# Kernel optimization log

Hardware: AMD Instinct MI355X
Metric: run time of the kernel (lower is better)

The kernel has to match this reference:

```python
import jax, jax.numpy as jnp
import numpy as np

DIM = 256          # inter_dim
GROUPS = 32        # GroupNorm groups
P = 8              # patch_size (square)
EPS = 1e-5


def group_norm(x, gamma, beta):
    # x: (b, c, h, w); normalize over (c/G, h, w) per group, biased variance (torch default)
    b, c, h, w = x.shape
    xg = x.reshape(b, GROUPS, -1)
    m = xg.mean(-1, keepdims=True)
    v = xg.var(-1, keepdims=True)
    xn = ((xg - m) * jax.lax.rsqrt(v + EPS)).reshape(b, c, h, w)
    return xn * gamma[None, :, None, None] + beta[None, :, None, None]


def to_patches(x):
    # 'b c (h p1) (w p2) -> (b h w) c (p1 p2)'
    b, c, H, W = x.shape
    nh, nw = H // P, W // P
    x = x.reshape(b, c, nh, P, nw, P).transpose(0, 2, 4, 1, 3, 5)  # b nh nw c p1 p2
    return x.reshape(b * nh * nw, c, P * P)


def from_patches(x, b, H, W):
    # '(b h w) c (p1 p2) -> b c (h p1) (w p2)'
    nh, nw = H // P, W // P
    c = x.shape[1]
    x = x.reshape(b, nh, nw, c, P, P).transpose(0, 3, 1, 4, 2, 5)
    return x.reshape(b, c, H, W)


def setup_inputs() -> dict:
    key = jax.random.key(0)
    ks = jax.random.split(key, 4)
    b, c, H, W = 8, 256, 128, 128
    return {
        "x_low": jax.random.normal(ks[0], (b, c, H, W), jnp.float32),
        "x_high": jax.random.normal(ks[1], (b, c, H, W), jnp.float32),
        "wq": jax.random.normal(ks[2], (DIM, c), jnp.float32) * (1.0 / np.sqrt(c)),
        "wk": jax.random.normal(ks[3], (DIM, c), jnp.float32) * (1.0 / np.sqrt(c)),
        "gq": jnp.ones((DIM,), jnp.float32),
        "bq": jnp.zeros((DIM,), jnp.float32),
        "gk": jnp.ones((DIM,), jnp.float32),
        "bk": jnp.zeros((DIM,), jnp.float32),
    }


def reference(x_low, x_high, wq, wk, gq, bq, gk, bk):
    b, c, H, W = x_low.shape
    # 1x1 conv (bias-free) + GroupNorm for q and k projections
    q = group_norm(jnp.einsum('oc,bchw->bohw', wq, x_low), gq, bq)
    k = group_norm(jnp.einsum('oc,bchw->bohw', wk, x_high), gk, bk)
    qp = to_patches(q).transpose(0, 2, 1)   # (n_windows, p, c)
    kp = to_patches(k)                      # (n_windows, c, p)
    attn = jax.nn.softmax(jnp.matmul(qp, kp) / jnp.sqrt(jnp.float32(DIM)), axis=-1)  # (n, p, p)
    out = jnp.matmul(attn, kp.transpose(0, 2, 1))  # (n, p, c)
    out = from_patches(out.transpose(0, 2, 1), b, H, W)
    return out + x_low
```

## Files before the change

### kernel.cpp

```cpp
#include <hip/hip_runtime.h>
#include <hip/hip_bf16.h>

using short8 = __attribute__((ext_vector_type(8))) short;
using fx4    = __attribute__((ext_vector_type(4))) float;

#define NB 8
#define CDIM 256
#define HH 128
#define NPIX 16384
#define NG_ELEMS 131072.0f

__device__ __forceinline__ float bf2f(short s) {
    union { unsigned u; float f; } c; c.u = ((unsigned)(unsigned short)s) << 16; return c.f;
}
__device__ __forceinline__ short f2bf(float f) {
    union { float f; unsigned u; } c; c.f = f;
    unsigned u = c.u;
    u += 0x7FFFu + ((u >> 16) & 1u);
    return (short)(u >> 16);
}
__device__ __forceinline__ short2 f2bf2(float a, float b) {
    __hip_bfloat162 h = __float22bfloat162_rn(make_float2(a, b));
    union { __hip_bfloat162 b; short2 s; } c; c.b = h; return c.s;
}

__global__ __launch_bounds__(256) void kW(const float* __restrict__ wq,
                                          const float* __restrict__ wk,
                                          short* __restrict__ WB) {
    int kc = blockIdx.x;
    int t  = blockIdx.y;
    const float* W = t ? wk : wq;
    int tid = threadIdx.x;
    int ntile = tid >> 4, lr = tid & 15;
    int n = ntile * 16 + lr;
#pragma unroll
    for (int quad = 0; quad < 4; ++quad) {
        const float* p = W + (size_t)n * CDIM + kc * 32 + quad * 8;
        fx4 v0 = *(const fx4*)p;
        fx4 v1 = *(const fx4*)(p + 4);
        union { short8 v; short2 h[4]; } s;
        s.h[0] = f2bf2(v0[0], v0[1]);
        s.h[1] = f2bf2(v0[2], v0[3]);
        s.h[2] = f2bf2(v1[0], v1[1]);
        s.h[3] = f2bf2(v1[2], v1[3]);
        *(short8*)(WB + ((((size_t)t * 8 + kc) * 16 + ntile) * 64 + quad * 16 + lr) * 8) = s.v;
    }
}

__global__ __launch_bounds__(256, 2) void kG(const float* __restrict__ xlo,
                                             const float* __restrict__ xhi,
                                             const short* __restrict__ WB,
                                             short* __restrict__ qt,
                                             short* __restrict__ kt,
                                             float* __restrict__ stats) {
    int m0 = blockIdx.x * 128;
    int zy = blockIdx.y;
    int b = zy >> 1, t = zy & 1;
    const float* X = (t ? xhi : xlo) + (size_t)b * CDIM * NPIX;
    const short* WBt = WB + (size_t)t * 8 * 16 * 64 * 8;
    short* OUT = (t ? kt : qt) + (size_t)b * NPIX * CDIM;
    int tid = threadIdx.x;
    int w = tid >> 6, l = tid & 63, lr = l & 15, quad = l >> 4;
    int mh = w >> 1, nh = w & 1;
    int pixb = m0 + mh * 64 + lr;

    fx4 acc[4][8];
#pragma unroll
    for (int mt = 0; mt < 4; ++mt)
#pragma unroll
        for (int nt = 0; nt < 8; ++nt) { acc[mt][nt][0]=0.f; acc[mt][nt][1]=0.f; acc[mt][nt][2]=0.f; acc[mt][nt][3]=0.f; }

    for (int kc = 0; kc < 8; ++kc) {
        short8 bf[8];
        const short* wb = WBt + ((size_t)kc * 16 + nh * 8) * 64 * 8 + (size_t)l * 8;
#pragma unroll
        for (int nt = 0; nt < 8; ++nt)
            bf[nt] = *(const short8*)(wb + (size_t)nt * 64 * 8);
        short8 af[4];
        const float* xp = X + (size_t)(kc * 32 + quad * 8) * NPIX + pixb;
#pragma unroll
        for (int mt = 0; mt < 4; ++mt) {
            float e0 = xp[(size_t)0 * NPIX + mt * 16];
            float e1 = xp[(size_t)1 * NPIX + mt * 16];
            float e2 = xp[(size_t)2 * NPIX + mt * 16];
            float e3 = xp[(size_t)3 * NPIX + mt * 16];
            float e4 = xp[(size_t)4 * NPIX + mt * 16];
            float e5 = xp[(size_t)5 * NPIX + mt * 16];
            float e6 = xp[(size_t)6 * NPIX + mt * 16];
            float e7 = xp[(size_t)7 * NPIX + mt * 16];
            union { short8 v; short2 h[4]; } s;
            s.h[0] = f2bf2(e0, e1); s.h[1] = f2bf2(e2, e3);
            s.h[2] = f2bf2(e4, e5); s.h[3] = f2bf2(e6, e7);
            af[mt] = s.v;
        }
#pragma unroll
        for (int mt = 0; mt < 4; ++mt)
#pragma unroll
            for (int nt = 0; nt < 8; ++nt)
                acc[mt][nt] = __builtin_amdgcn_mfma_f32_16x16x32_bf16(af[mt], bf[nt], acc[mt][nt], 0, 0, 0);
    }

#pragma unroll
    for (int nt = 0; nt < 8; ++nt) {
        float s = 0.f, ss = 0.f;
#pragma unroll
        for (int mt = 0; mt < 4; ++mt)
#pragma unroll
            for (int r = 0; r < 4; ++r) { float v = acc[mt][nt][r]; s += v; ss += v * v; }
        s += __shfl_xor(s, 16); ss += __shfl_xor(ss, 16);
        s += __shfl_xor(s, 32); ss += __shfl_xor(ss, 32);
        s += __shfl_xor(s, 1);  ss += __shfl_xor(ss, 1);
        s += __shfl_xor(s, 2);  ss += __shfl_xor(ss, 2);
        s += __shfl_xor(s, 4);  ss += __shfl_xor(ss, 4);
        if (l == 0 || l == 8) {
            int o = nh * 128 + nt * 16 + (l & 15);
            int g = o >> 3;
            float* st = stats + ((size_t)(t * NB + b) * 32 + g) * 2;
            atomicAdd(st, s);
            atomicAdd(st + 1, ss);
        }
    }

#pragma unroll
    for (int mt = 0; mt < 4; ++mt) {
        int pix = m0 + mh * 64 + mt * 16 + quad * 4;
#pragma unroll
        for (int nt = 0; nt < 8; ++nt) {
            int o = nh * 128 + nt * 16 + lr;
            short2 p0 = f2bf2(acc[mt][nt][0], acc[mt][nt][1]);
            short2 p1 = f2bf2(acc[mt][nt][2], acc[mt][nt][3]);
            OUT[(size_t)(pix + 0) * CDIM + o] = p0.x;
            OUT[(size_t)(pix + 1) * CDIM + o] = p0.y;
            OUT[(size_t)(pix + 2) * CDIM + o] = p1.x;
            OUT[(size_t)(pix + 3) * CDIM + o] = p1.y;
        }
    }
}

__global__ __launch_bounds__(256) void kS(const float* __restrict__ stats,
                                          const float* __restrict__ gq,
                                          const float* __restrict__ bq,
                                          const float* __restrict__ gk,
                                          const float* __restrict__ bk,
                                          float* __restrict__ scale,
                                          float* __restrict__ shift) {
    int id = blockIdx.x * 256 + threadIdx.x;
    int t = id >> 11, b = (id >> 8) & 7, o = id & 255;
    int g = o >> 3;
    const float* st = stats + ((size_t)(t * NB + b) * 32 + g) * 2;
    float mean = st[0] * (1.0f / NG_ELEMS);
    float var  = st[1] * (1.0f / NG_ELEMS) - mean * mean;
    float rstd = rsqrtf(var + 1e-5f);
    float gamma = (t ? gk : gq)[o];
    float beta  = (t ? bk : bq)[o];
    float sc = gamma * rstd;
    scale[id] = sc;
    shift[id] = beta - mean * sc;
}

__global__ __launch_bounds__(256) void kA(const short* __restrict__ qt,
                                          const short* __restrict__ kt,
                                          const float* __restrict__ scale,
                                          const float* __restrict__ shift,
                                          const float* __restrict__ xlo,
                                          float* __restrict__ outp) {
    __shared__ short Ks[64 * 264];
    __shared__ float SsF[64 * 68];
    __shared__ short Ps[64 * 72];
    short* Os = (short*)SsF;

    int blk = blockIdx.x;
    int b = blk >> 8, wh = (blk >> 4) & 15, ww = blk & 15;
    int tid = threadIdx.x;
    int w = tid >> 6, l = tid & 63, lr = l & 15, quad = l >> 4;

    const float* sq = scale + (size_t)b * CDIM;
    const float* zq = shift + (size_t)b * CDIM;
    const float* sk = scale + (size_t)(NB + b) * CDIM;
    const float* zk = shift + (size_t)(NB + b) * CDIM;

    {
        int oct = tid & 31;
        int j00 = tid >> 5;
        float skv[8], zkv[8];
#pragma unroll
        for (int e = 0; e < 8; ++e) { skv[e] = sk[oct * 8 + e]; zkv[e] = zk[oct * 8 + e]; }
#pragma unroll
        for (int it = 0; it < 8; ++it) {
            int j = j00 + it * 8;
            int pix = (wh * 8 + (j >> 3)) * HH + ww * 8 + (j & 7);
            short8 kv = *(const short8*)(kt + ((size_t)b * NPIX + pix) * CDIM + oct * 8);
            short8 nv;
#pragma unroll
            for (int e = 0; e < 8; ++e) nv[e] = f2bf(bf2f(kv[e]) * skv[e] + zkv[e]);
            *(short8*)(&Ks[j * 264 + oct * 8]) = nv;
        }
    }
    __syncthreads();

    {
        fx4 accS[4];
#pragma unroll
        for (int nt = 0; nt < 4; ++nt) { accS[nt][0]=0.f; accS[nt][1]=0.f; accS[nt][2]=0.f; accS[nt][3]=0.f; }
        int qi = 16 * w + lr;
        int pixq = (wh * 8 + (qi >> 3)) * HH + ww * 8 + (qi & 7);
        const short* qrow = qt + ((size_t)b * NPIX + pixq) * CDIM;
#pragma unroll
        for (int kc = 0; kc < 8; ++kc) {
            int c0 = kc * 32 + quad * 8;
            short8 qv = *(const short8*)(qrow + c0);
            short8 aq;
#pragma unroll
            for (int e = 0; e < 8; ++e) aq[e] = f2bf(bf2f(qv[e]) * sq[c0 + e] + zq[c0 + e]);
#pragma unroll
            for (int nt = 0; nt < 4; ++nt) {
                short8 bk8 = *(const short8*)(&Ks[(nt * 16 + lr) * 264 + c0]);
                accS[nt] = __builtin_amdgcn_mfma_f32_16x16x32_bf16(aq, bk8, accS[nt], 0, 0, 0);
            }
        }
#pragma unroll
        for (int nt = 0; nt < 4; ++nt)
#pragma unroll
            for (int r = 0; r < 4; ++r)
                SsF[(16 * w + quad * 4 + r) * 68 + nt * 16 + lr] = accS[nt][r] * 0.0625f;
    }
    __syncthreads();

    {
        int row = tid >> 2, seg = tid & 3;
        float v[16];
#pragma unroll
        for (int k4 = 0; k4 < 4; ++k4) {
            fx4 t4 = *(const fx4*)(&SsF[row * 68 + seg * 16 + k4 * 4]);
            v[k4*4+0] = t4[0]; v[k4*4+1] = t4[1]; v[k4*4+2] = t4[2]; v[k4*4+3] = t4[3];
        }
        float m = v[0];
#pragma unroll
        for (int e = 1; e < 16; ++e) m = fmaxf(m, v[e]);
        m = fmaxf(m, __shfl_xor(m, 1));
        m = fmaxf(m, __shfl_xor(m, 2));
        float s = 0.f;
#pragma unroll
        for (int e = 0; e < 16; ++e) { v[e] = __expf(v[e] - m); s += v[e]; }
        s += __shfl_xor(s, 1);
        s += __shfl_xor(s, 2);
        float inv = 1.0f / s;
        short8 p0, p1;
#pragma unroll
        for (int e = 0; e < 8; ++e) { p0[e] = f2bf(v[e] * inv); p1[e] = f2bf(v[8 + e] * inv); }
        *(short8*)(&Ps[row * 72 + seg * 16]) = p0;
        *(short8*)(&Ps[row * 72 + seg * 16 + 8]) = p1;
    }
    __syncthreads();

    fx4 accO[4][4];
#pragma unroll
    for (int mt = 0; mt < 4; ++mt)
#pragma unroll
        for (int nt = 0; nt < 4; ++nt) { accO[mt][nt][0]=0.f; accO[mt][nt][1]=0.f; accO[mt][nt][2]=0.f; accO[mt][nt][3]=0.f; }
#pragma unroll
    for (int kc2 = 0; kc2 < 2; ++kc2) {
        int j0 = kc2 * 32 + quad * 8;
        short8 ap[4];
#pragma unroll
        for (int mt = 0; mt < 4; ++mt)
            ap[mt] = *(const short8*)(&Ps[(mt * 16 + lr) * 72 + j0]);
#pragma unroll
        for (int nt = 0; nt < 4; ++nt) {
            int c = 64 * w + nt * 16 + lr;
            short8 bk8;
#pragma unroll
            for (int jj = 0; jj < 8; ++jj) bk8[jj] = Ks[(j0 + jj) * 264 + c];
#pragma unroll
            for (int mt = 0; mt < 4; ++mt)
                accO[mt][nt] = __builtin_amdgcn_mfma_f32_16x16x32_bf16(ap[mt], bk8, accO[mt][nt], 0, 0, 0);
        }
    }

    int half = w >> 1;
#pragma unroll
    for (int h2 = 0; h2 < 2; ++h2) {
        __syncthreads();
        if (half == h2) {
#pragma unroll
            for (int mt = 0; mt < 4; ++mt)
#pragma unroll
                for (int nt = 0; nt < 4; ++nt) {
                    int i = mt * 16 + quad * 4;
                    int cl = 64 * w + nt * 16 + lr - 128 * h2;
#pragma unroll
                    for (int r = 0; r < 4; ++r)
                        Os[(i + r) * 136 + cl] = f2bf(accO[mt][nt][r]);
                }
        }
        __syncthreads();
#pragma unroll
        for (int it = 0; it < 4; ++it) {
            int id = tid + it * 256;
            int cl = id & 127, h = id >> 7;
            int cg = cl + 128 * h2;
            size_t gidx = ((size_t)(b * CDIM + cg)) * NPIX + (size_t)(wh * 8 + h) * HH + ww * 8;
            fx4 x0 = *(const fx4*)(xlo + gidx);
            fx4 x1 = *(const fx4*)(xlo + gidx + 4);
            fx4 r0, r1;
#pragma unroll
            for (int jj = 0; jj < 4; ++jj) {
                r0[jj] = bf2f(Os[(h * 8 + jj)     * 136 + cl]) + x0[jj];
                r1[jj] = bf2f(Os[(h * 8 + 4 + jj) * 136 + cl]) + x1[jj];
            }
            *(fx4*)(outp + gidx)     = r0;
            *(fx4*)(outp + gidx + 4) = r1;
        }
    }
}

extern "C" void kernel_launch(void* const* d_in, const int* in_sizes, int n_in,
                              void* d_out, int out_size, void* d_ws, size_t ws_size,
                              hipStream_t stream) {
    const float* xlo = (const float*)d_in[0];
    const float* xhi = (const float*)d_in[1];
    const float* wqp = (const float*)d_in[2];
    const float* wkp = (const float*)d_in[3];
    const float* gq  = (const float*)d_in[4];
    const float* bq  = (const float*)d_in[5];
    const float* gk  = (const float*)d_in[6];
    const float* bk  = (const float*)d_in[7];
    float* outp = (float*)d_out;
    char* ws = (char*)d_ws;
    size_t SZB = (size_t)NB * NPIX * CDIM * 2;
    short* qt    = (short*)(ws);
    short* kt    = (short*)(ws + SZB);
    float* stats = (float*)(ws + 2 * SZB);
    float* scale = (float*)(ws + 2 * SZB + 4096);
    float* shift = (float*)(ws + 2 * SZB + 4096 + 16384);
    short* WB    = (short*)(ws + 2 * SZB + 4096 + 32768);

    hipMemsetAsync(stats, 0, 4096, stream);
    kW<<<dim3(8, 2), dim3(256), 0, stream>>>(wqp, wkp, WB);
    kG<<<dim3(128, 16), dim3(256), 0, stream>>>(xlo, xhi, WB, qt, kt, stats);
    kS<<<dim3(16), dim3(256), 0, stream>>>(stats, gq, bq, gk, bk, scale, shift);
    kA<<<dim3(2048), dim3(256), 0, stream>>>(qt, kt, scale, shift, xlo, outp);
}
```

Baseline: 621.6 us.

## Restructure projection GEMM with swapped operands, register prefetch, and vectorized stores

The 1x1-conv projection kernel now uses 64-pixel tiles with each wave owning 64 output channels. Weights become the MFMA A operand so that accumulator rows map to channels. The next K-chunk of activations is gathered into a double-buffered register array while the current chunk is converted and multiplied. This lets each lane write four contiguous bf16 channels as one vector store instead of four scattered 2-byte stores. The aim is to hide global load latency and cut store transactions, at the cost of more registers, twice as many blocks, and more atomics for the GroupNorm statistics.

```diff
diff --git a/kernel.cpp b/kernel.cpp
--- a/kernel.cpp
+++ b/kernel.cpp
@@ -1,8 +1,9 @@
 #include <hip/hip_runtime.h>
 #include <hip/hip_bf16.h>
 
-using short8 = __attribute__((ext_vector_type(8))) short;
-using fx4    = __attribute__((ext_vector_type(4))) float;
+using short8  = __attribute__((ext_vector_type(8))) short;
+using short4v = __attribute__((ext_vector_type(4))) short;
+using fx4     = __attribute__((ext_vector_type(4))) float;
 
 #define NB 8
 #define CDIM 256
@@ -47,13 +48,40 @@
     }
 }
 
+
+#define GATHER(BUF, KCV) do {                                                      \
+    const float* xp_ = X + (size_t)((KCV) * 32 + quad * 8) * NPIX + m0 + lr;       \
+    _Pragma("unroll") for (int pt_ = 0; pt_ < 4; ++pt_)                            \
+    _Pragma("unroll") for (int e_ = 0; e_ < 8; ++e_)                               \
+        BUF[pt_ * 8 + e_] = xp_[(size_t)e_ * NPIX + pt_ * 16];                     \
+} while (0)
+
+#define STEP(CUR, NXT, KCV, PF) do {                                               \
+    short8 af_[4];                                                                 \
+    const short* wb_ = WBt + (((size_t)(KCV) * 16 + w * 4) * 64 + l) * 8;          \
+    _Pragma("unroll") for (int m_ = 0; m_ < 4; ++m_)                               \
+        af_[m_] = *(const short8*)(wb_ + (size_t)m_ * 64 * 8);                     \
+    if (PF) { GATHER(NXT, (KCV) + 1); }                                            \
+    short8 bf_[4];                                                                 \
+    _Pragma("unroll") for (int pt_ = 0; pt_ < 4; ++pt_) {                          \
+        union { short8 v; short2 h[4]; } s_;                                       \
+        _Pragma("unroll") for (int j_ = 0; j_ < 4; ++j_)                           \
+            s_.h[j_] = f2bf2(CUR[pt_ * 8 + 2 * j_], CUR[pt_ * 8 + 2 * j_ + 1]);    \
+        bf_[pt_] = s_.v;                                                           \
+    }                                                                              \
+    _Pragma("unroll") for (int m_ = 0; m_ < 4; ++m_)                               \
+    _Pragma("unroll") for (int pt_ = 0; pt_ < 4; ++pt_)                            \
+        acc[m_][pt_] = __builtin_amdgcn_mfma_f32_16x16x32_bf16(af_[m_], bf_[pt_],  \
+                                                               acc[m_][pt_], 0, 0, 0); \
+} while (0)
+
 __global__ __launch_bounds__(256, 2) void kG(const float* __restrict__ xlo,
                                              const float* __restrict__ xhi,
                                              const short* __restrict__ WB,
                                              short* __restrict__ qt,
                                              short* __restrict__ kt,
                                              float* __restrict__ stats) {
-    int m0 = blockIdx.x * 128;
+    int m0 = blockIdx.x * 64;
     int zy = blockIdx.y;
     int b = zy >> 1, t = zy & 1;
     const float* X = (t ? xhi : xlo) + (size_t)b * CDIM * NPIX;
@@ -61,78 +89,64 @@
     short* OUT = (t ? kt : qt) + (size_t)b * NPIX * CDIM;
     int tid = threadIdx.x;
     int w = tid >> 6, l = tid & 63, lr = l & 15, quad = l >> 4;
-    int mh = w >> 1, nh = w & 1;
-    int pixb = m0 + mh * 64 + lr;
-
-    fx4 acc[4][8];
-#pragma unroll
-    for (int mt = 0; mt < 4; ++mt)
-#pragma unroll
-        for (int nt = 0; nt < 8; ++nt) { acc[mt][nt][0]=0.f; acc[mt][nt][1]=0.f; acc[mt][nt][2]=0.f; acc[mt][nt][3]=0.f; }
-
-    for (int kc = 0; kc < 8; ++kc) {
-        short8 bf[8];
-        const short* wb = WBt + ((size_t)kc * 16 + nh * 8) * 64 * 8 + (size_t)l * 8;
-#pragma unroll
-        for (int nt = 0; nt < 8; ++nt)
-            bf[nt] = *(const short8*)(wb + (size_t)nt * 64 * 8);
-        short8 af[4];
-        const float* xp = X + (size_t)(kc * 32 + quad * 8) * NPIX + pixb;
-#pragma unroll
-        for (int mt = 0; mt < 4; ++mt) {
-            float e0 = xp[(size_t)0 * NPIX + mt * 16];
-            float e1 = xp[(size_t)1 * NPIX + mt * 16];
-            float e2 = xp[(size_t)2 * NPIX + mt * 16];
-            float e3 = xp[(size_t)3 * NPIX + mt * 16];
-            float e4 = xp[(size_t)4 * NPIX + mt * 16];
-            float e5 = xp[(size_t)5 * NPIX + mt * 16];
-            float e6 = xp[(size_t)6 * NPIX + mt * 16];
-            float e7 = xp[(size_t)7 * NPIX + mt * 16];
-            union { short8 v; short2 h[4]; } s;
-            s.h[0] = f2bf2(e0, e1); s.h[1] = f2bf2(e2, e3);
-            s.h[2] = f2bf2(e4, e5); s.h[3] = f2bf2(e6, e7);
-            af[mt] = s.v;
-        }
-#pragma unroll
-        for (int mt = 0; mt < 4; ++mt)
-#pragma unroll
-            for (int nt = 0; nt < 8; ++nt)
-                acc[mt][nt] = __builtin_amdgcn_mfma_f32_16x16x32_bf16(af[mt], bf[nt], acc[mt][nt], 0, 0, 0);
-    }
-
-#pragma unroll
-    for (int nt = 0; nt < 8; ++nt) {
-        float s = 0.f, ss = 0.f;
-#pragma unroll
-        for (int mt = 0; mt < 4; ++mt)
-#pragma unroll
-            for (int r = 0; r < 4; ++r) { float v = acc[mt][nt][r]; s += v; ss += v * v; }
-        s += __shfl_xor(s, 16); ss += __shfl_xor(ss, 16);
-        s += __shfl_xor(s, 32); ss += __shfl_xor(ss, 32);
-        s += __shfl_xor(s, 1);  ss += __shfl_xor(ss, 1);
-        s += __shfl_xor(s, 2);  ss += __shfl_xor(ss, 2);
-        s += __shfl_xor(s, 4);  ss += __shfl_xor(ss, 4);
-        if (l == 0 || l == 8) {
-            int o = nh * 128 + nt * 16 + (l & 15);
-            int g = o >> 3;
-            float* st = stats + ((size_t)(t * NB + b) * 32 + g) * 2;
-            atomicAdd(st, s);
-            atomicAdd(st + 1, ss);
-        }
-    }
-
-#pragma unroll
-    for (int mt = 0; mt < 4; ++mt) {
-        int pix = m0 + mh * 64 + mt * 16 + quad * 4;
-#pragma unroll
-        for (int nt = 0; nt < 8; ++nt) {
-            int o = nh * 128 + nt * 16 + lr;
-            short2 p0 = f2bf2(acc[mt][nt][0], acc[mt][nt][1]);
-            short2 p1 = f2bf2(acc[mt][nt][2], acc[mt][nt][3]);
-            OUT[(size_t)(pix + 0) * CDIM + o] = p0.x;
-            OUT[(size_t)(pix + 1) * CDIM + o] = p0.y;
-            OUT[(size_t)(pix + 2) * CDIM + o] = p1.x;
-            OUT[(size_t)(pix + 3) * CDIM + o] = p1.y;
+
+    fx4 acc[4][4];
+#pragma unroll
+    for (int m = 0; m < 4; ++m)
+#pragma unroll
+        for (int n = 0; n < 4; ++n) { acc[m][n][0]=0.f; acc[m][n][1]=0.f; acc[m][n][2]=0.f; acc[m][n][3]=0.f; }
+
+    float pfA[32], pfB[32];
+
+    GATHER(pfA, 0);
+    STEP(pfA, pfB, 0, 1);
+    STEP(pfB, pfA, 1, 1);
+    STEP(pfA, pfB, 2, 1);
+    STEP(pfB, pfA, 3, 1);
+    STEP(pfA, pfB, 4, 1);
+    STEP(pfB, pfA, 5, 1);
+    STEP(pfA, pfB, 6, 1);
+    STEP(pfB, pfA, 7, 0);
+
+    {
+        float s[4][4], ss[4][4];
+#pragma unroll
+        for (int m = 0; m < 4; ++m)
+#pragma unroll
+            for (int r = 0; r < 4; ++r) {
+                float a0 = acc[m][0][r], a1 = acc[m][1][r], a2 = acc[m][2][r], a3 = acc[m][3][r];
+                s[m][r]  = (a0 + a1) + (a2 + a3);
+                ss[m][r] = (a0 * a0 + a1 * a1) + (a2 * a2 + a3 * a3);
+            }
+#pragma unroll
+        for (int m = 0; m < 4; ++m)
+#pragma unroll
+            for (int r = 0; r < 4; ++r) {
+                float sv = s[m][r], sq = ss[m][r];
+                sv += __shfl_xor(sv, 1);  sq += __shfl_xor(sq, 1);
+                sv += __shfl_xor(sv, 2);  sq += __shfl_xor(sq, 2);
+                sv += __shfl_xor(sv, 4);  sq += __shfl_xor(sq, 4);
+                sv += __shfl_xor(sv, 8);  sq += __shfl_xor(sq, 8);
+                if (lr == 0) {
+                    int o = w * 64 + m * 16 + quad * 4 + r;
+                    int g = o >> 3;
+                    float* st = stats + ((size_t)(t * NB + b) * 32 + g) * 2;
+                    atomicAdd(st, sv);
+                    atomicAdd(st + 1, sq);
+                }
+            }
+    }
+
+#pragma unroll
+    for (int n = 0; n < 4; ++n) {
+        int pix = m0 + n * 16 + lr;
+        short* op = OUT + (size_t)pix * CDIM + w * 64 + quad * 4;
+#pragma unroll
+        for (int m = 0; m < 4; ++m) {
+            short2 p0 = f2bf2(acc[m][n][0], acc[m][n][1]);
+            short2 p1 = f2bf2(acc[m][n][2], acc[m][n][3]);
+            short4v v; v[0] = p0.x; v[1] = p0.y; v[2] = p1.x; v[3] = p1.y;
+            *(short4v*)(op + m * 16) = v;
         }
     }
 }
@@ -337,7 +351,7 @@
 
     hipMemsetAsync(stats, 0, 4096, stream);
     kW<<<dim3(8, 2), dim3(256), 0, stream>>>(wqp, wkp, WB);
-    kG<<<dim3(128, 16), dim3(256), 0, stream>>>(xlo, xhi, WB, qt, kt, stats);
+    kG<<<dim3(256, 16), dim3(256), 0, stream>>>(xlo, xhi, WB, qt, kt, stats);
     kS<<<dim3(16), dim3(256), 0, stream>>>(stats, gq, bq, gk, bk, scale, shift);
     kA<<<dim3(2048), dim3(256), 0, stream>>>(qt, kt, scale, shift, xlo, outp);
 }
```

New measurement: 2.267 ms. 3.65x slower.
